# Optimization experiments

Hardware: AMD Instinct MI355X
Metric: run time of the kernel (lower is better)

## Reference

```python
import jax, jax.numpy as jnp
import numpy as np

B, T, C, H = 2, 2048, 1024, 16
HS = C // H

def setup_inputs() -> dict:
    key = jax.random.key(0)
    ks = jax.random.split(key, 5)
    s = 0.02
    return {
        "x": jax.random.normal(ks[0], (B, T, C), jnp.float32),
        "W_attn": jax.random.normal(ks[1], (C, 3 * C), jnp.float32) * s,
        "b_attn": jax.random.normal(ks[2], (3 * C,), jnp.float32) * s,
        "W_proj": jax.random.normal(ks[3], (C, C), jnp.float32) * s,
        "b_proj": jax.random.normal(ks[4], (C,), jnp.float32) * s,
    }

def reference(x, W_attn, b_attn, W_proj, b_proj):
    qkv = x @ W_attn + b_attn                      # [B,T,3C]
    q, k, v = jnp.split(qkv, 3, axis=-1)
    # [B,T,C] -> [B,H,T,hs]
    def heads(t):
        return t.reshape(B, T, H, HS).transpose(0, 2, 1, 3)
    q, k, v = heads(q), heads(k), heads(v)
    scale = 1.0 / jnp.sqrt(jnp.asarray(HS, x.dtype))
    attn = jnp.einsum('bhqd,bhkd->bhqk', q, k) * scale
    causal = jnp.tril(jnp.ones((T, T), bool))
    attn = jnp.where(causal[None, None], attn, -jnp.inf)
    attn = jax.nn.softmax(attn, axis=-1)
    y = jnp.einsum('bhqk,bhkd->bhqd', attn, v)
    y = y.transpose(0, 2, 1, 3).reshape(B, T, C)
    return y @ W_proj + b_proj
```

## Files before the change

### kernel.cpp

```cpp
#include <hip/hip_runtime.h>
#include <hip/hip_bf16.h>

static constexpr int Bn = 2, Tn = 2048, Cn = 1024, Hn = 16, HSn = 64;
static constexpr int Mrows = Bn * Tn;
static constexpr size_t PL = (size_t)Bn * Hn * Tn * HSn;

typedef __attribute__((ext_vector_type(8))) short short8;
typedef __attribute__((ext_vector_type(4))) float f32x4;

__device__ __forceinline__ unsigned short f2bf(float f) {
  __hip_bfloat16 h = __float2bfloat16(f);
  return *reinterpret_cast<unsigned short*>(&h);
}

__device__ __forceinline__ float fexp2(float x) {
  return __builtin_amdgcn_exp2f(x);
}

__device__ __forceinline__ void gload_lds16(const void* g, void* l) {
  __builtin_amdgcn_global_load_lds(
      (const __attribute__((address_space(1))) void*)g,
      (__attribute__((address_space(3))) void*)l, 16, 0, 0);
}

#define QSC 0.18033688011112042591999058512524f

__global__ __launch_bounds__(256) void prep_all(
    const float* __restrict__ x, unsigned short* __restrict__ xb,
    const float* __restrict__ Wa, unsigned short* __restrict__ Wab,
    const float* __restrict__ Wp, unsigned short* __restrict__ Wpb)
{
  const int bid = blockIdx.x, tid = threadIdx.x;
  if (bid < 4096) {
    int i = bid * 256 + tid;
    float4 v = ((const float4*)x)[i];
    ushort4 o;
    o.x = f2bf(v.x); o.y = f2bf(v.y); o.z = f2bf(v.z); o.w = f2bf(v.w);
    ((ushort4*)xb)[i] = o;
    return;
  }
  __shared__ float tile[32][33];
  const float* src; unsigned short* dst; int R, Cc, tb;
  if (bid < 4096 + 3072) { src = Wa; dst = Wab; R = Cn; Cc = 3 * Cn; tb = bid - 4096; }
  else                   { src = Wp; dst = Wpb; R = Cn; Cc = Cn;     tb = bid - 4096 - 3072; }
  const int nbx = Cc / 32;
  const int bx = tb % nbx, by = tb / nbx;
  const int tx = tid & 31, ty = tid >> 5;
  const int c0 = bx * 32, r0 = by * 32;
  #pragma unroll
  for (int i = 0; i < 4; ++i)
    tile[ty + 8 * i][tx] = src[(size_t)(r0 + ty + 8 * i) * Cc + c0 + tx];
  __syncthreads();
  #pragma unroll
  for (int i = 0; i < 4; ++i)
    dst[(size_t)(c0 + ty + 8 * i) * R + r0 + tx] = f2bf(tile[tx][ty + 8 * i]);
}

__global__ __launch_bounds__(512) void gemmQKV(
    const unsigned short* __restrict__ A, const unsigned short* __restrict__ Bt,
    const float* __restrict__ bias, unsigned short* __restrict__ qkv, int K)
{
  constexpr int NSTEP = 1024 / 64;
  constexpr int AF = 32;
  constexpr int BF = 24;
  __shared__ alignas(16) unsigned char lds[2][(AF + BF) * 1024];

  const int tid = threadIdx.x, wave = tid >> 6, lane = tid & 63;
  const int wr = wave >> 2, wc = wave & 3;
  const int orig = blockIdx.x;
  const int swz = (orig & 7) * 32 + (orig >> 3);
  const int bx = swz & 15, by = swz >> 4;
  const int tM = by * 256, tN = bx * 192;

  auto STAGE = [&](int buf, int k0) {
    #pragma unroll
    for (int i = 0; i < 7; ++i) {
      int f = wave * 7 + i;
      const unsigned short* g;
      int off;
      if (f < AF) {
        int mg = f >> 1, ks = f & 1;
        g = A + (size_t)(tM + mg * 16 + (lane & 15)) * K + k0 + ks * 32 + (lane >> 4) * 8;
        off = f * 1024;
      } else {
        int fg = f - AF;
        int ng = fg >> 1, ks = fg & 1;
        g = Bt + (size_t)(tN + ng * 16 + (lane & 15)) * K + k0 + ks * 32 + (lane >> 4) * 8;
        off = AF * 1024 + fg * 1024;
      }
      gload_lds16(g, &lds[buf][off]);
    }
  };

  f32x4 acc[8][3] = {};

  STAGE(0, 0);
  STAGE(1, 64);

  for (int t = 0; t < NSTEP; ++t) {
    if (t == NSTEP - 1)
      asm volatile("s_waitcnt vmcnt(0)" ::: "memory");
    else
      asm volatile("s_waitcnt vmcnt(7)" ::: "memory");
    __builtin_amdgcn_s_barrier();

    const int cur = t & 1;
    short8 af[8][2], bfr[3][2];
    #pragma unroll
    for (int ks = 0; ks < 2; ++ks) {
      #pragma unroll
      for (int m = 0; m < 8; ++m)
        af[m][ks] = *(const short8*)&lds[cur][((wr * 8 + m) * 2 + ks) * 1024 + lane * 16];
      #pragma unroll
      for (int n = 0; n < 3; ++n)
        bfr[n][ks] = *(const short8*)&lds[cur][AF * 1024 + ((wc * 3 + n) * 2 + ks) * 1024 + lane * 16];
    }
    asm volatile("s_waitcnt lgkmcnt(0)" ::: "memory");
    __builtin_amdgcn_sched_barrier(0);
    __builtin_amdgcn_s_barrier();

    if (t + 2 < NSTEP) STAGE(cur, (t + 2) * 64);

    __builtin_amdgcn_s_setprio(1);
    #pragma unroll
    for (int ks = 0; ks < 2; ++ks)
      #pragma unroll
      for (int m = 0; m < 8; ++m)
        #pragma unroll
        for (int n = 0; n < 3; ++n)
          acc[m][n] = __builtin_amdgcn_mfma_f32_16x16x32_bf16(af[m][ks], bfr[n][ks], acc[m][n], 0, 0, 0);
    __builtin_amdgcn_s_setprio(0);
  }

  const int a = lane & 15, hq = lane >> 4;
  #pragma unroll
  for (int m = 0; m < 8; ++m) {
    #pragma unroll
    for (int n = 0; n < 3; ++n) {
      int c = tN + wc * 48 + n * 16 + a;
      float bv = bias[c];
      int which = c >> 10;
      int cc = c & 1023, hh = cc >> 6, d = cc & 63;
      int row0 = tM + wr * 128 + m * 16 + hq * 4;
      int b = row0 >> 11, t0 = row0 & 2047;
      int bh = b * Hn + hh;
      if (which == 2) {
        ushort4 pk;
        pk.x = f2bf(acc[m][n][0] + bv);
        pk.y = f2bf(acc[m][n][1] + bv);
        pk.z = f2bf(acc[m][n][2] + bv);
        pk.w = f2bf(acc[m][n][3] + bv);
        *(ushort4*)&qkv[2 * PL + ((size_t)bh * HSn + d) * Tn + t0] = pk;
      } else {
        float sc = (which == 0) ? QSC : 1.0f;
        #pragma unroll
        for (int r = 0; r < 4; ++r) {
          float v = (acc[m][n][r] + bv) * sc;
          qkv[(size_t)which * PL + ((size_t)bh * Tn + t0 + r) * HSn + d] = f2bf(v);
        }
      }
    }
  }
}

template <int WM, int WN>
__global__ __launch_bounds__(256) void gemmP(
    const unsigned short* __restrict__ A, const unsigned short* __restrict__ Bt,
    const float* __restrict__ bias, float* __restrict__ O, int N, int K)
{
  constexpr int BM = WM * 32, BNt = WN * 32;
  constexpr int AF = BM / 16;
  constexpr int BF = BNt / 16;
  constexpr int NF = AF + BF;
  constexpr int PW = NF / 4;
  static_assert(PW == 3, "vmcnt literal");
  __shared__ alignas(16) unsigned char lds[2][NF * 1024];

  const int tid = threadIdx.x, wave = tid >> 6, lane = tid & 63;
  const int wr = wave >> 1, wc = wave & 1;
  const int orig = blockIdx.x;
  const int swz = (orig & 7) * 64 + (orig >> 3);
  const int bx = swz & 15, by = swz >> 4;
  const int tM = by * BM, tN = bx * BNt;

  auto STAGE = [&](int buf, int k0) {
    #pragma unroll
    for (int i = 0; i < PW; ++i) {
      int f = wave * PW + i;
      const unsigned short* g;
      if (f < AF)
        g = A + (size_t)(tM + f * 16 + (lane & 15)) * K + k0 + (lane >> 4) * 8;
      else
        g = Bt + (size_t)(tN + (f - AF) * 16 + (lane & 15)) * K + k0 + (lane >> 4) * 8;
      gload_lds16(g, &lds[buf][f * 1024]);
    }
  };

  f32x4 acc[WM][WN] = {};

  STAGE(0, 0);
  for (int t = 0, k0 = 0;; ++t, k0 += 32) {
    const int cur = t & 1;
    if (k0 + 32 < K) {
      STAGE(cur ^ 1, k0 + 32);
      asm volatile("s_waitcnt vmcnt(3)" ::: "memory");
    } else {
      asm volatile("s_waitcnt vmcnt(0)" ::: "memory");
    }
    __builtin_amdgcn_s_barrier();

    short8 af[WM], bfr[WN];
    #pragma unroll
    for (int m = 0; m < WM; ++m)
      af[m] = *(const short8*)&lds[cur][(wr * WM + m) * 1024 + lane * 16];
    #pragma unroll
    for (int n = 0; n < WN; ++n)
      bfr[n] = *(const short8*)&lds[cur][(AF + wc * WN + n) * 1024 + lane * 16];
    #pragma unroll
    for (int m = 0; m < WM; ++m)
      #pragma unroll
      for (int n = 0; n < WN; ++n)
        acc[m][n] = __builtin_amdgcn_mfma_f32_16x16x32_bf16(af[m], bfr[n], acc[m][n], 0, 0, 0);

    __builtin_amdgcn_s_barrier();
    if (k0 + 32 >= K) break;
  }

  const int a = lane & 15, hq = lane >> 4;
  #pragma unroll
  for (int m = 0; m < WM; ++m) {
    #pragma unroll
    for (int n = 0; n < WN; ++n) {
      int c = tN + wc * (WN * 16) + n * 16 + a;
      float bv = bias[c];
      int r0 = tM + wr * (WM * 16) + m * 16 + hq * 4;
      #pragma unroll
      for (int r = 0; r < 4; ++r)
        O[(size_t)(r0 + r) * N + c] = acc[m][n][r] + bv;
    }
  }
}

__global__ __launch_bounds__(256) void attn_mfma(
    const unsigned short* __restrict__ Qg, const unsigned short* __restrict__ Kg,
    const unsigned short* __restrict__ Vtg, unsigned short* __restrict__ Y)
{
  __shared__ alignas(16) unsigned char lds[41984];
  const int flat = blockIdx.x;
  const int logical = (flat & 7) * 64 + (flat >> 3);
  const int bh = logical >> 4;
  const int yb = logical & 15;
  const int tid = threadIdx.x, wave = tid >> 6, lane = tid & 63;
  const int a = lane & 15, h = lane >> 4;
  const unsigned short* Qp = Qg + (size_t)bh * Tn * HSn;
  const unsigned short* Kp = Kg + (size_t)bh * Tn * HSn;
  const unsigned short* Vp = Vtg + (size_t)bh * HSn * Tn;
  const int pbase = wave * 2304;
  const int qglob = wave * 16 + a;
  const int b = bh >> 4, hd = bh & 15;

  auto STAGE_K = [&](int kb, int kv0) {
    #pragma unroll
    for (int i = 0; i < 2; ++i) {
      int r8 = wave * 16 + i * 8;
      int row = r8 + (lane >> 3);
      int ch = (lane & 7) ^ (row & 7);
      gload_lds16(Kp + (size_t)(kv0 + row) * HSn + ch * 8,
                  &lds[9216 + kb * 8192 + r8 * 128]);
    }
  };
  auto STAGE_V = [&](int vb, int kv0) {
    #pragma unroll
    for (int i = 0; i < 2; ++i) {
      int r8 = wave * 16 + i * 8;
      int row = r8 + (lane >> 3);
      int ch = (lane & 7) ^ (row & 7);
      gload_lds16(Vp + (size_t)row * Tn + kv0 + ch * 8,
                  &lds[25600 + vb * 8192 + r8 * 128]);
    }
  };

  short8 ones;
  #pragma unroll
  for (int j = 0; j < 8; ++j) ones[j] = (short)0x3F80;

  for (int ph = 0; ph < 2; ++ph) {
    const int qt = ph ? (31 - yb) : yb;
    const int q0 = qt * 64;

    short8 qf[2];
    #pragma unroll
    for (int ks = 0; ks < 2; ++ks)
      qf[ks] = *(const short8*)(Qp + (size_t)(q0 + qglob) * HSn + ks * 32 + h * 8);

    STAGE_K(0, 0);
    STAGE_V(0, 0);
    if (qt >= 1) {
      STAGE_K(1, 64);
      STAGE_V(1, 64);
    }

    f32x4 o[4] = {};
    f32x4 lacc = {};

    for (int t = 0; t <= qt; ++t) {
      const int kb = t & 1;
      if (t == qt)
        asm volatile("s_waitcnt vmcnt(0)" ::: "memory");
      else
        asm volatile("s_waitcnt vmcnt(4)" ::: "memory");
      __builtin_amdgcn_s_barrier();

      const int kbase = 9216 + kb * 8192;
      const int vbase = 25600 + kb * 8192;

      f32x4 s[4] = {};
      __builtin_amdgcn_s_setprio(1);
      #pragma unroll
      for (int ks = 0; ks < 2; ++ks)
        #pragma unroll
        for (int n = 0; n < 4; ++n) {
          int kr = n * 16 + a;
          int ch = (ks * 4 + h) ^ (kr & 7);
          short8 kf = *(const short8*)&lds[kbase + kr * 128 + ch * 16];
          s[n] = __builtin_amdgcn_mfma_f32_16x16x32_bf16(kf, qf[ks], s[n], 0, 0, 0);
        }
      __builtin_amdgcn_s_setprio(0);

      if (t == qt) {
        #pragma unroll
        for (int n = 0; n < 4; ++n)
          #pragma unroll
          for (int r = 0; r < 4; ++r)
            if ((n * 16 + h * 4 + r) > qglob) s[n][r] = -1e30f;
      }

      #pragma unroll
      for (int n = 0; n < 4; ++n)
        #pragma unroll
        for (int r = 0; r < 4; ++r) s[n][r] = fexp2(s[n][r]);

      #pragma unroll
      for (int n = 0; n < 4; ++n) {
        uint2 w2;
        w2.x = (unsigned)f2bf(s[n][0]) | ((unsigned)f2bf(s[n][1]) << 16);
        w2.y = (unsigned)f2bf(s[n][2]) | ((unsigned)f2bf(s[n][3]) << 16);
        *(uint2*)&lds[pbase + (a * 36 + n * 8 + h * 2) * 4] = w2;
      }

      __builtin_amdgcn_s_setprio(1);
      #pragma unroll
      for (int ks = 0; ks < 2; ++ks) {
        short8 pa = *(const short8*)&lds[pbase + (a * 36 + ks * 16 + h * 4) * 4];
        lacc = __builtin_amdgcn_mfma_f32_16x16x32_bf16(pa, ones, lacc, 0, 0, 0);
        #pragma unroll
        for (int n = 0; n < 4; ++n) {
          int d = n * 16 + a;
          int ch = (ks * 4 + h) ^ (d & 7);
          short8 vf = *(const short8*)&lds[vbase + d * 128 + ch * 16];
          o[n] = __builtin_amdgcn_mfma_f32_16x16x32_bf16(pa, vf, o[n], 0, 0, 0);
        }
      }
      __builtin_amdgcn_s_setprio(0);

      __builtin_amdgcn_s_barrier();
      if (t + 2 <= qt) {
        STAGE_K(kb, (t + 2) * 64);
        STAGE_V(kb, (t + 2) * 64);
      }
    }

    f32x4 inv;
    #pragma unroll
    for (int r = 0; r < 4; ++r) inv[r] = 1.0f / lacc[r];
    #pragma unroll
    for (int n = 0; n < 4; ++n)
      #pragma unroll
      for (int r = 0; r < 4; ++r) {
        int tr = q0 + wave * 16 + 4 * h + r;
        int col = hd * 64 + n * 16 + a;
        Y[((size_t)(b * Tn + tr)) * Cn + col] = f2bf(o[n][r] * inv[r]);
      }
  }
}

extern "C" void kernel_launch(void* const* d_in, const int* in_sizes, int n_in,
                              void* d_out, int out_size, void* d_ws, size_t ws_size,
                              hipStream_t stream) {
  const float* x      = (const float*)d_in[0];
  const float* W_attn = (const float*)d_in[1];
  const float* b_attn = (const float*)d_in[2];
  const float* W_proj = (const float*)d_in[3];
  const float* b_proj = (const float*)d_in[4];
  float* out = (float*)d_out;

  unsigned short* xb  = (unsigned short*)d_ws;
  unsigned short* Wab = xb + (size_t)Mrows * Cn;
  unsigned short* Wpb = Wab + (size_t)3 * Cn * Cn;
  unsigned short* qkv = Wpb + (size_t)Cn * Cn;
  unsigned short* y   = qkv + 3 * PL;

  prep_all<<<4096 + 3072 + 1024, 256, 0, stream>>>(x, xb, W_attn, Wab, W_proj, Wpb);

  gemmQKV<<<256, 512, 0, stream>>>(xb, Wab, b_attn, qkv, Cn);

  attn_mfma<<<512, 256, 0, stream>>>(qkv, qkv + PL, qkv + 2 * PL, y);

  gemmP<4, 2><<<512, 256, 0, stream>>>(y, Wpb, b_proj, out, Cn, Cn);
}
```

Before: 109.3 us.

## Fuse all four stages into one persistent kernel with grid barriers

Replaces the four separate launches (conversion/transpose, QKV GEMM, attention, projection GEMM) with a single persistent kernel of 256 blocks of 512 threads, separated by software grid barriers built on atomics. Attention and projection stages pack two former 256-thread blocks into each 512-thread block using separate LDS halves. The aim is to remove kernel launch gaps and tail effects between stages. In exchange it adds a memset launch, spin-wait barriers that rely on all 256 blocks being co-resident, and only one block per CU via launch bounds and large LDS, which may reduce latency hiding in the attention and projection phases.

New measurement: 390.3 us. 257% more time.

```diff
diff --git a/kernel.cpp b/kernel.cpp
--- a/kernel.cpp
+++ b/kernel.cpp
@@ -25,362 +25,372 @@
 
 #define QSC 0.18033688011112042591999058512524f
 
-__global__ __launch_bounds__(256) void prep_all(
-    const float* __restrict__ x, unsigned short* __restrict__ xb,
-    const float* __restrict__ Wa, unsigned short* __restrict__ Wab,
-    const float* __restrict__ Wp, unsigned short* __restrict__ Wpb)
+__device__ __forceinline__ void grid_barrier(unsigned* bar, int slot) {
+  __threadfence();
+  __syncthreads();
+  if (threadIdx.x == 0) {
+    atomicAdd(&bar[slot], 1u);
+    while (atomicAdd(&bar[slot], 0u) < 256u) __builtin_amdgcn_s_sleep(8);
+  }
+  __syncthreads();
+  __threadfence();
+}
+
+__global__ __launch_bounds__(512, 1) void fused_all(
+    const float* __restrict__ x,
+    const float* __restrict__ Wa, const float* __restrict__ ba,
+    const float* __restrict__ Wp, const float* __restrict__ bp,
+    unsigned short* __restrict__ xb, unsigned short* __restrict__ Wab,
+    unsigned short* __restrict__ Wpb, unsigned short* __restrict__ qkv,
+    unsigned short* __restrict__ y, float* __restrict__ out,
+    unsigned* __restrict__ bar)
 {
-  const int bid = blockIdx.x, tid = threadIdx.x;
-  if (bid < 4096) {
-    int i = bid * 256 + tid;
-    float4 v = ((const float4*)x)[i];
-    ushort4 o;
-    o.x = f2bf(v.x); o.y = f2bf(v.y); o.z = f2bf(v.z); o.w = f2bf(v.w);
-    ((ushort4*)xb)[i] = o;
-    return;
+  __shared__ alignas(16) unsigned char lds[114688];
+  const int blk = blockIdx.x, tid = threadIdx.x;
+  const int wave = tid >> 6, lane = tid & 63;
+  const int a = lane & 15, h = lane >> 4;
+
+  {
+    const float4* xs = (const float4*)x;
+    ushort4* xd = (ushort4*)xb;
+    for (int i = blk * 512 + tid; i < Mrows * Cn / 4; i += 256 * 512) {
+      float4 v = xs[i];
+      ushort4 o;
+      o.x = f2bf(v.x); o.y = f2bf(v.y); o.z = f2bf(v.z); o.w = f2bf(v.w);
+      xd[i] = o;
+    }
+    float* tile = (float*)(lds + (tid >> 8) * 4224);
+    const int t256 = tid & 255;
+    const int tx = t256 & 31, ty = t256 >> 5;
+    for (int pass = 0; pass < 8; ++pass) {
+      int tb = blk * 16 + pass * 2 + (tid >> 8);
+      const float* src; unsigned short* dst; int Cc, tnum;
+      if (tb < 3072) { src = Wa; dst = Wab; Cc = 3 * Cn; tnum = tb; }
+      else           { src = Wp; dst = Wpb; Cc = Cn;     tnum = tb - 3072; }
+      const int nbx = Cc / 32;
+      const int bx = tnum % nbx, by = tnum / nbx;
+      const int c0 = bx * 32, r0 = by * 32;
+      #pragma unroll
+      for (int i = 0; i < 4; ++i)
+        tile[(ty + 8 * i) * 33 + tx] = src[(size_t)(r0 + ty + 8 * i) * Cc + c0 + tx];
+      __syncthreads();
+      #pragma unroll
+      for (int i = 0; i < 4; ++i)
+        dst[(size_t)(c0 + ty + 8 * i) * Cn + r0 + tx] = f2bf(tile[tx * 33 + ty + 8 * i]);
+      __syncthreads();
+    }
   }
-  __shared__ float tile[32][33];
-  const float* src; unsigned short* dst; int R, Cc, tb;
-  if (bid < 4096 + 3072) { src = Wa; dst = Wab; R = Cn; Cc = 3 * Cn; tb = bid - 4096; }
-  else                   { src = Wp; dst = Wpb; R = Cn; Cc = Cn;     tb = bid - 4096 - 3072; }
-  const int nbx = Cc / 32;
-  const int bx = tb % nbx, by = tb / nbx;
-  const int tx = tid & 31, ty = tid >> 5;
-  const int c0 = bx * 32, r0 = by * 32;
-  #pragma unroll
-  for (int i = 0; i < 4; ++i)
-    tile[ty + 8 * i][tx] = src[(size_t)(r0 + ty + 8 * i) * Cc + c0 + tx];
-  __syncthreads();
-  #pragma unroll
-  for (int i = 0; i < 4; ++i)
-    dst[(size_t)(c0 + ty + 8 * i) * R + r0 + tx] = f2bf(tile[tx][ty + 8 * i]);
-}
-
-__global__ __launch_bounds__(512) void gemmQKV(
-    const unsigned short* __restrict__ A, const unsigned short* __restrict__ Bt,
-    const float* __restrict__ bias, unsigned short* __restrict__ qkv, int K)
-{
-  constexpr int NSTEP = 1024 / 64;
-  constexpr int AF = 32;
-  constexpr int BF = 24;
-  __shared__ alignas(16) unsigned char lds[2][(AF + BF) * 1024];
-
-  const int tid = threadIdx.x, wave = tid >> 6, lane = tid & 63;
-  const int wr = wave >> 2, wc = wave & 3;
-  const int orig = blockIdx.x;
-  const int swz = (orig & 7) * 32 + (orig >> 3);
-  const int bx = swz & 15, by = swz >> 4;
-  const int tM = by * 256, tN = bx * 192;
-
-  auto STAGE = [&](int buf, int k0) {
-    #pragma unroll
-    for (int i = 0; i < 7; ++i) {
-      int f = wave * 7 + i;
-      const unsigned short* g;
-      int off;
-      if (f < AF) {
-        int mg = f >> 1, ks = f & 1;
-        g = A + (size_t)(tM + mg * 16 + (lane & 15)) * K + k0 + ks * 32 + (lane >> 4) * 8;
-        off = f * 1024;
-      } else {
-        int fg = f - AF;
-        int ng = fg >> 1, ks = fg & 1;
-        g = Bt + (size_t)(tN + ng * 16 + (lane & 15)) * K + k0 + ks * 32 + (lane >> 4) * 8;
-        off = AF * 1024 + fg * 1024;
-      }
-      gload_lds16(g, &lds[buf][off]);
-    }
-  };
-
-  f32x4 acc[8][3] = {};
-
-  STAGE(0, 0);
-  STAGE(1, 64);
-
-  for (int t = 0; t < NSTEP; ++t) {
-    if (t == NSTEP - 1)
-      asm volatile("s_waitcnt vmcnt(0)" ::: "memory");
-    else
-      asm volatile("s_waitcnt vmcnt(7)" ::: "memory");
-    __builtin_amdgcn_s_barrier();
-
-    const int cur = t & 1;
-    short8 af[8][2], bfr[3][2];
-    #pragma unroll
-    for (int ks = 0; ks < 2; ++ks) {
-      #pragma unroll
-      for (int m = 0; m < 8; ++m)
-        af[m][ks] = *(const short8*)&lds[cur][((wr * 8 + m) * 2 + ks) * 1024 + lane * 16];
-      #pragma unroll
-      for (int n = 0; n < 3; ++n)
-        bfr[n][ks] = *(const short8*)&lds[cur][AF * 1024 + ((wc * 3 + n) * 2 + ks) * 1024 + lane * 16];
-    }
-    asm volatile("s_waitcnt lgkmcnt(0)" ::: "memory");
-    __builtin_amdgcn_sched_barrier(0);
-    __builtin_amdgcn_s_barrier();
-
-    if (t + 2 < NSTEP) STAGE(cur, (t + 2) * 64);
-
-    __builtin_amdgcn_s_setprio(1);
-    #pragma unroll
-    for (int ks = 0; ks < 2; ++ks)
-      #pragma unroll
-      for (int m = 0; m < 8; ++m)
-        #pragma unroll
-        for (int n = 0; n < 3; ++n)
-          acc[m][n] = __builtin_amdgcn_mfma_f32_16x16x32_bf16(af[m][ks], bfr[n][ks], acc[m][n], 0, 0, 0);
-    __builtin_amdgcn_s_setprio(0);
-  }
-
-  const int a = lane & 15, hq = lane >> 4;
-  #pragma unroll
-  for (int m = 0; m < 8; ++m) {
-    #pragma unroll
-    for (int n = 0; n < 3; ++n) {
-      int c = tN + wc * 48 + n * 16 + a;
-      float bv = bias[c];
-      int which = c >> 10;
-      int cc = c & 1023, hh = cc >> 6, d = cc & 63;
-      int row0 = tM + wr * 128 + m * 16 + hq * 4;
-      int b = row0 >> 11, t0 = row0 & 2047;
-      int bh = b * Hn + hh;
-      if (which == 2) {
-        ushort4 pk;
-        pk.x = f2bf(acc[m][n][0] + bv);
-        pk.y = f2bf(acc[m][n][1] + bv);
-        pk.z = f2bf(acc[m][n][2] + bv);
-        pk.w = f2bf(acc[m][n][3] + bv);
-        *(ushort4*)&qkv[2 * PL + ((size_t)bh * HSn + d) * Tn + t0] = pk;
-      } else {
-        float sc = (which == 0) ? QSC : 1.0f;
-        #pragma unroll
-        for (int r = 0; r < 4; ++r) {
-          float v = (acc[m][n][r] + bv) * sc;
-          qkv[(size_t)which * PL + ((size_t)bh * Tn + t0 + r) * HSn + d] = f2bf(v);
-        }
-      }
-    }
-  }
-}
-
-template <int WM, int WN>
-__global__ __launch_bounds__(256) void gemmP(
-    const unsigned short* __restrict__ A, const unsigned short* __restrict__ Bt,
-    const float* __restrict__ bias, float* __restrict__ O, int N, int K)
-{
-  constexpr int BM = WM * 32, BNt = WN * 32;
-  constexpr int AF = BM / 16;
-  constexpr int BF = BNt / 16;
-  constexpr int NF = AF + BF;
-  constexpr int PW = NF / 4;
-  static_assert(PW == 3, "vmcnt literal");
-  __shared__ alignas(16) unsigned char lds[2][NF * 1024];
-
-  const int tid = threadIdx.x, wave = tid >> 6, lane = tid & 63;
-  const int wr = wave >> 1, wc = wave & 1;
-  const int orig = blockIdx.x;
-  const int swz = (orig & 7) * 64 + (orig >> 3);
-  const int bx = swz & 15, by = swz >> 4;
-  const int tM = by * BM, tN = bx * BNt;
-
-  auto STAGE = [&](int buf, int k0) {
-    #pragma unroll
-    for (int i = 0; i < PW; ++i) {
-      int f = wave * PW + i;
-      const unsigned short* g;
-      if (f < AF)
-        g = A + (size_t)(tM + f * 16 + (lane & 15)) * K + k0 + (lane >> 4) * 8;
-      else
-        g = Bt + (size_t)(tN + (f - AF) * 16 + (lane & 15)) * K + k0 + (lane >> 4) * 8;
-      gload_lds16(g, &lds[buf][f * 1024]);
-    }
-  };
-
-  f32x4 acc[WM][WN] = {};
-
-  STAGE(0, 0);
-  for (int t = 0, k0 = 0;; ++t, k0 += 32) {
-    const int cur = t & 1;
-    if (k0 + 32 < K) {
-      STAGE(cur ^ 1, k0 + 32);
-      asm volatile("s_waitcnt vmcnt(3)" ::: "memory");
-    } else {
-      asm volatile("s_waitcnt vmcnt(0)" ::: "memory");
-    }
-    __builtin_amdgcn_s_barrier();
-
-    short8 af[WM], bfr[WN];
-    #pragma unroll
-    for (int m = 0; m < WM; ++m)
-      af[m] = *(const short8*)&lds[cur][(wr * WM + m) * 1024 + lane * 16];
-    #pragma unroll
-    for (int n = 0; n < WN; ++n)
-      bfr[n] = *(const short8*)&lds[cur][(AF + wc * WN + n) * 1024 + lane * 16];
-    #pragma unroll
-    for (int m = 0; m < WM; ++m)
-      #pragma unroll
-      for (int n = 0; n < WN; ++n)
-        acc[m][n] = __builtin_amdgcn_mfma_f32_16x16x32_bf16(af[m], bfr[n], acc[m][n], 0, 0, 0);
-
-    __builtin_amdgcn_s_barrier();
-    if (k0 + 32 >= K) break;
-  }
-
-  const int a = lane & 15, hq = lane >> 4;
-  #pragma unroll
-  for (int m = 0; m < WM; ++m) {
-    #pragma unroll
-    for (int n = 0; n < WN; ++n) {
-      int c = tN + wc * (WN * 16) + n * 16 + a;
-      float bv = bias[c];
-      int r0 = tM + wr * (WM * 16) + m * 16 + hq * 4;
-      #pragma unroll
-      for (int r = 0; r < 4; ++r)
-        O[(size_t)(r0 + r) * N + c] = acc[m][n][r] + bv;
-    }
-  }
-}
-
-__global__ __launch_bounds__(256) void attn_mfma(
-    const unsigned short* __restrict__ Qg, const unsigned short* __restrict__ Kg,
-    const unsigned short* __restrict__ Vtg, unsigned short* __restrict__ Y)
-{
-  __shared__ alignas(16) unsigned char lds[41984];
-  const int flat = blockIdx.x;
-  const int logical = (flat & 7) * 64 + (flat >> 3);
-  const int bh = logical >> 4;
-  const int yb = logical & 15;
-  const int tid = threadIdx.x, wave = tid >> 6, lane = tid & 63;
-  const int a = lane & 15, h = lane >> 4;
-  const unsigned short* Qp = Qg + (size_t)bh * Tn * HSn;
-  const unsigned short* Kp = Kg + (size_t)bh * Tn * HSn;
-  const unsigned short* Vp = Vtg + (size_t)bh * HSn * Tn;
-  const int pbase = wave * 2304;
-  const int qglob = wave * 16 + a;
-  const int b = bh >> 4, hd = bh & 15;
-
-  auto STAGE_K = [&](int kb, int kv0) {
-    #pragma unroll
-    for (int i = 0; i < 2; ++i) {
-      int r8 = wave * 16 + i * 8;
-      int row = r8 + (lane >> 3);
-      int ch = (lane & 7) ^ (row & 7);
-      gload_lds16(Kp + (size_t)(kv0 + row) * HSn + ch * 8,
-                  &lds[9216 + kb * 8192 + r8 * 128]);
-    }
-  };
-  auto STAGE_V = [&](int vb, int kv0) {
-    #pragma unroll
-    for (int i = 0; i < 2; ++i) {
-      int r8 = wave * 16 + i * 8;
-      int row = r8 + (lane >> 3);
-      int ch = (lane & 7) ^ (row & 7);
-      gload_lds16(Vp + (size_t)row * Tn + kv0 + ch * 8,
-                  &lds[25600 + vb * 8192 + r8 * 128]);
-    }
-  };
-
-  short8 ones;
-  #pragma unroll
-  for (int j = 0; j < 8; ++j) ones[j] = (short)0x3F80;
-
-  for (int ph = 0; ph < 2; ++ph) {
-    const int qt = ph ? (31 - yb) : yb;
-    const int q0 = qt * 64;
-
-    short8 qf[2];
-    #pragma unroll
-    for (int ks = 0; ks < 2; ++ks)
-      qf[ks] = *(const short8*)(Qp + (size_t)(q0 + qglob) * HSn + ks * 32 + h * 8);
-
-    STAGE_K(0, 0);
-    STAGE_V(0, 0);
-    if (qt >= 1) {
-      STAGE_K(1, 64);
-      STAGE_V(1, 64);
-    }
-
-    f32x4 o[4] = {};
-    f32x4 lacc = {};
-
-    for (int t = 0; t <= qt; ++t) {
-      const int kb = t & 1;
-      if (t == qt)
+  grid_barrier(bar, 0);
+
+  {
+    constexpr int NSTEP = 16;
+    constexpr int AF = 32, BF = 24;
+    const int wr = wave >> 2, wc = wave & 3;
+    const int swz = (blk & 7) * 32 + (blk >> 3);
+    const int bx = swz & 15, by = swz >> 4;
+    const int tM = by * 256, tN = bx * 192;
+    const int K = Cn;
+
+    auto STAGE = [&](int buf, int k0) {
+      #pragma unroll
+      for (int i = 0; i < 7; ++i) {
+        int f = wave * 7 + i;
+        const unsigned short* g;
+        int off;
+        if (f < AF) {
+          int mg = f >> 1, ks = f & 1;
+          g = xb + (size_t)(tM + mg * 16 + (lane & 15)) * K + k0 + ks * 32 + (lane >> 4) * 8;
+          off = f * 1024;
+        } else {
+          int fg = f - AF;
+          int ng = fg >> 1, ks = fg & 1;
+          g = Wab + (size_t)(tN + ng * 16 + (lane & 15)) * K + k0 + ks * 32 + (lane >> 4) * 8;
+          off = AF * 1024 + fg * 1024;
+        }
+        gload_lds16(g, &lds[buf * 57344 + off]);
+      }
+    };
+
+    f32x4 acc[8][3] = {};
+
+    STAGE(0, 0);
+    STAGE(1, 64);
+
+    for (int t = 0; t < NSTEP; ++t) {
+      if (t == NSTEP - 1)
         asm volatile("s_waitcnt vmcnt(0)" ::: "memory");
       else
-        asm volatile("s_waitcnt vmcnt(4)" ::: "memory");
+        asm volatile("s_waitcnt vmcnt(7)" ::: "memory");
       __builtin_amdgcn_s_barrier();
 
-      const int kbase = 9216 + kb * 8192;
-      const int vbase = 25600 + kb * 8192;
-
-      f32x4 s[4] = {};
+      const int cur = t & 1;
+      const unsigned char* base = &lds[cur * 57344];
+      short8 af[8][2], bfr[3][2];
+      #pragma unroll
+      for (int ks = 0; ks < 2; ++ks) {
+        #pragma unroll
+        for (int m = 0; m < 8; ++m)
+          af[m][ks] = *(const short8*)&base[((wr * 8 + m) * 2 + ks) * 1024 + lane * 16];
+        #pragma unroll
+        for (int n = 0; n < 3; ++n)
+          bfr[n][ks] = *(const short8*)&base[AF * 1024 + ((wc * 3 + n) * 2 + ks) * 1024 + lane * 16];
+      }
+      asm volatile("s_waitcnt lgkmcnt(0)" ::: "memory");
+      __builtin_amdgcn_sched_barrier(0);
+      __builtin_amdgcn_s_barrier();
+
+      if (t + 2 < NSTEP) STAGE(cur, (t + 2) * 64);
+
       __builtin_amdgcn_s_setprio(1);
       #pragma unroll
       for (int ks = 0; ks < 2; ++ks)
         #pragma unroll
+        for (int m = 0; m < 8; ++m)
+          #pragma unroll
+          for (int n = 0; n < 3; ++n)
+            acc[m][n] = __builtin_amdgcn_mfma_f32_16x16x32_bf16(af[m][ks], bfr[n][ks], acc[m][n], 0, 0, 0);
+      __builtin_amdgcn_s_setprio(0);
+    }
+
+    const int hq = lane >> 4;
+    #pragma unroll
+    for (int m = 0; m < 8; ++m) {
+      #pragma unroll
+      for (int n = 0; n < 3; ++n) {
+        int c = tN + wc * 48 + n * 16 + a;
+        float bv = ba[c];
+        int which = c >> 10;
+        int cc = c & 1023, hh = cc >> 6, d = cc & 63;
+        int row0 = tM + wr * 128 + m * 16 + hq * 4;
+        int b = row0 >> 11, t0 = row0 & 2047;
+        int bh = b * Hn + hh;
+        if (which == 2) {
+          ushort4 pk;
+          pk.x = f2bf(acc[m][n][0] + bv);
+          pk.y = f2bf(acc[m][n][1] + bv);
+          pk.z = f2bf(acc[m][n][2] + bv);
+          pk.w = f2bf(acc[m][n][3] + bv);
+          *(ushort4*)&qkv[2 * PL + ((size_t)bh * HSn + d) * Tn + t0] = pk;
+        } else {
+          float sc = (which == 0) ? QSC : 1.0f;
+          #pragma unroll
+          for (int r = 0; r < 4; ++r) {
+            float v = (acc[m][n][r] + bv) * sc;
+            qkv[(size_t)which * PL + ((size_t)bh * Tn + t0 + r) * HSn + d] = f2bf(v);
+          }
+        }
+      }
+    }
+  }
+  grid_barrier(bar, 1);
+
+  {
+    const int yb = blk & 15;
+    const int half = wave >> 2;
+    const int bh = ((blk >> 4) << 1) | half;
+    const int w4 = wave & 3;
+    unsigned char* L = lds + half * 41984;
+    const unsigned short* Qp = qkv + (size_t)bh * Tn * HSn;
+    const unsigned short* Kp = qkv + PL + (size_t)bh * Tn * HSn;
+    const unsigned short* Vp = qkv + 2 * PL + (size_t)bh * HSn * Tn;
+    const int pbase = w4 * 2304;
+    const int qglob = w4 * 16 + a;
+    const int b = bh >> 4, hd = bh & 15;
+
+    auto STAGE_K = [&](int kb, int kv0) {
+      #pragma unroll
+      for (int i = 0; i < 2; ++i) {
+        int r8 = w4 * 16 + i * 8;
+        int row = r8 + (lane >> 3);
+        int ch = (lane & 7) ^ (row & 7);
+        gload_lds16(Kp + (size_t)(kv0 + row) * HSn + ch * 8,
+                    &L[9216 + kb * 8192 + r8 * 128]);
+      }
+    };
+    auto STAGE_V = [&](int vb, int kv0) {
+      #pragma unroll
+      for (int i = 0; i < 2; ++i) {
+        int r8 = w4 * 16 + i * 8;
+        int row = r8 + (lane >> 3);
+        int ch = (lane & 7) ^ (row & 7);
+        gload_lds16(Vp + (size_t)row * Tn + kv0 + ch * 8,
+                    &L[25600 + vb * 8192 + r8 * 128]);
+      }
+    };
+
+    short8 ones;
+    #pragma unroll
+    for (int j = 0; j < 8; ++j) ones[j] = (short)0x3F80;
+
+    for (int ph = 0; ph < 2; ++ph) {
+      const int qt = ph ? (31 - yb) : yb;
+      const int q0 = qt * 64;
+
+      short8 qf[2];
+      #pragma unroll
+      for (int ks = 0; ks < 2; ++ks)
+        qf[ks] = *(const short8*)(Qp + (size_t)(q0 + qglob) * HSn + ks * 32 + h * 8);
+
+      STAGE_K(0, 0);
+      STAGE_V(0, 0);
+      if (qt >= 1) {
+        STAGE_K(1, 64);
+        STAGE_V(1, 64);
+      }
+
+      f32x4 o[4] = {};
+      f32x4 lacc = {};
+
+      for (int t = 0; t <= qt; ++t) {
+        const int kb = t & 1;
+        if (t == qt)
+          asm volatile("s_waitcnt vmcnt(0)" ::: "memory");
+        else
+          asm volatile("s_waitcnt vmcnt(4)" ::: "memory");
+        __builtin_amdgcn_s_barrier();
+
+        const int kbase = 9216 + kb * 8192;
+        const int vbase = 25600 + kb * 8192;
+
+        f32x4 s[4] = {};
+        __builtin_amdgcn_s_setprio(1);
+        #pragma unroll
+        for (int ks = 0; ks < 2; ++ks)
+          #pragma unroll
+          for (int n = 0; n < 4; ++n) {
+            int kr = n * 16 + a;
+            int ch = (ks * 4 + h) ^ (kr & 7);
+            short8 kf = *(const short8*)&L[kbase + kr * 128 + ch * 16];
+            s[n] = __builtin_amdgcn_mfma_f32_16x16x32_bf16(kf, qf[ks], s[n], 0, 0, 0);
+          }
+        __builtin_amdgcn_s_setprio(0);
+
+        if (t == qt) {
+          #pragma unroll
+          for (int n = 0; n < 4; ++n)
+            #pragma unroll
+            for (int r = 0; r < 4; ++r)
+              if ((n * 16 + h * 4 + r) > qglob) s[n][r] = -1e30f;
+        }
+
+        #pragma unroll
+        for (int n = 0; n < 4; ++n)
+          #pragma unroll
+          for (int r = 0; r < 4; ++r) s[n][r] = fexp2(s[n][r]);
+
+        #pragma unroll
         for (int n = 0; n < 4; ++n) {
-          int kr = n * 16 + a;
-          int ch = (ks * 4 + h) ^ (kr & 7);
-          short8 kf = *(const short8*)&lds[kbase + kr * 128 + ch * 16];
-          s[n] = __builtin_amdgcn_mfma_f32_16x16x32_bf16(kf, qf[ks], s[n], 0, 0, 0);
-        }
-      __builtin_amdgcn_s_setprio(0);
-
-      if (t == qt) {
-        #pragma unroll
-        for (int n = 0; n < 4; ++n)
-          #pragma unroll
-          for (int r = 0; r < 4; ++r)
-            if ((n * 16 + h * 4 + r) > qglob) s[n][r] = -1e30f;
-      }
-
+          uint2 w2;
+          w2.x = (unsigned)f2bf(s[n][0]) | ((unsigned)f2bf(s[n][1]) << 16);
+          w2.y = (unsigned)f2bf(s[n][2]) | ((unsigned)f2bf(s[n][3]) << 16);
+          *(uint2*)&L[pbase + (a * 36 + n * 8 + h * 2) * 4] = w2;
+        }
+
+        __builtin_amdgcn_s_setprio(1);
+        #pragma unroll
+        for (int ks = 0; ks < 2; ++ks) {
+          short8 pa = *(const short8*)&L[pbase + (a * 36 + ks * 16 + h * 4) * 4];
+          lacc = __builtin_amdgcn_mfma_f32_16x16x32_bf16(pa, ones, lacc, 0, 0, 0);
+          #pragma unroll
+          for (int n = 0; n < 4; ++n) {
+            int d = n * 16 + a;
+            int ch = (ks * 4 + h) ^ (d & 7);
+            short8 vf = *(const short8*)&L[vbase + d * 128 + ch * 16];
+            o[n] = __builtin_amdgcn_mfma_f32_16x16x32_bf16(pa, vf, o[n], 0, 0, 0);
+          }
+        }
+        __builtin_amdgcn_s_setprio(0);
+
+        __builtin_amdgcn_s_barrier();
+        if (t + 2 <= qt) {
+          STAGE_K(kb, (t + 2) * 64);
+          STAGE_V(kb, (t + 2) * 64);
+        }
+      }
+
+      f32x4 inv;
+      #pragma unroll
+      for (int r = 0; r < 4; ++r) inv[r] = 1.0f / lacc[r];
       #pragma unroll
       for (int n = 0; n < 4; ++n)
         #pragma unroll
-        for (int r = 0; r < 4; ++r) s[n][r] = fexp2(s[n][r]);
-
-      #pragma unroll
-      for (int n = 0; n < 4; ++n) {
-        uint2 w2;
-        w2.x = (unsigned)f2bf(s[n][0]) | ((unsigned)f2bf(s[n][1]) << 16);
-        w2.y = (unsigned)f2bf(s[n][2]) | ((unsigned)f2bf(s[n][3]) << 16);
-        *(uint2*)&lds[pbase + (a * 36 + n * 8 + h * 2) * 4] = w2;
-      }
-
-      __builtin_amdgcn_s_setprio(1);
-      #pragma unroll
-      for (int ks = 0; ks < 2; ++ks) {
-        short8 pa = *(const short8*)&lds[pbase + (a * 36 + ks * 16 + h * 4) * 4];
-        lacc = __builtin_amdgcn_mfma_f32_16x16x32_bf16(pa, ones, lacc, 0, 0, 0);
-        #pragma unroll
-        for (int n = 0; n < 4; ++n) {
-          int d = n * 16 + a;
-          int ch = (ks * 4 + h) ^ (d & 7);
-          short8 vf = *(const short8*)&lds[vbase + d * 128 + ch * 16];
-          o[n] = __builtin_amdgcn_mfma_f32_16x16x32_bf16(pa, vf, o[n], 0, 0, 0);
-        }
-      }
-      __builtin_amdgcn_s_setprio(0);
-
+        for (int r = 0; r < 4; ++r) {
+          int tr = q0 + w4 * 16 + 4 * h + r;
+          int col = hd * 64 + n * 16 + a;
+          y[((size_t)(b * Tn + tr)) * Cn + col] = f2bf(o[n][r] * inv[r]);
+        }
+    }
+  }
+  grid_barrier(bar, 2);
+
+  {
+    constexpr int AF = 8, BF = 4;
+    const int bx = blk & 15;
+    const int half = wave >> 2;
+    const int by = ((blk >> 4) << 1) | half;
+    const int w4 = wave & 3;
+    const int wr = w4 >> 1, wc = w4 & 1;
+    unsigned char* L = lds + half * 24576;
+    const int tM = by * 128, tN = bx * 64;
+    const int K = Cn;
+
+    auto STAGE = [&](int buf, int k0) {
+      #pragma unroll
+      for (int i = 0; i < 3; ++i) {
+        int f = w4 * 3 + i;
+        const unsigned short* g;
+        if (f < AF)
+          g = y + (size_t)(tM + f * 16 + (lane & 15)) * K + k0 + (lane >> 4) * 8;
+        else
+          g = Wpb + (size_t)(tN + (f - AF) * 16 + (lane & 15)) * K + k0 + (lane >> 4) * 8;
+        gload_lds16(g, &L[buf * 12288 + f * 1024]);
+      }
+    };
+
+    f32x4 acc[4][2] = {};
+
+    STAGE(0, 0);
+    for (int t = 0, k0 = 0;; ++t, k0 += 32) {
+      const int cur = t & 1;
+      if (k0 + 32 < K) {
+        STAGE(cur ^ 1, k0 + 32);
+        asm volatile("s_waitcnt vmcnt(3)" ::: "memory");
+      } else {
+        asm volatile("s_waitcnt vmcnt(0)" ::: "memory");
+      }
       __builtin_amdgcn_s_barrier();
-      if (t + 2 <= qt) {
-        STAGE_K(kb, (t + 2) * 64);
-        STAGE_V(kb, (t + 2) * 64);
-      }
-    }
-
-    f32x4 inv;
+
+      const unsigned char* base = &L[cur * 12288];
+      short8 af[4], bfr[2];
+      #pragma unroll
+      for (int m = 0; m < 4; ++m)
+        af[m] = *(const short8*)&base[(wr * 4 + m) * 1024 + lane * 16];
+      #pragma unroll
+      for (int n = 0; n < 2; ++n)
+        bfr[n] = *(const short8*)&base[(AF + wc * 2 + n) * 1024 + lane * 16];
+      #pragma unroll
+      for (int m = 0; m < 4; ++m)
+        #pragma unroll
+        for (int n = 0; n < 2; ++n)
+          acc[m][n] = __builtin_amdgcn_mfma_f32_16x16x32_bf16(af[m], bfr[n], acc[m][n], 0, 0, 0);
+
+      __builtin_amdgcn_s_barrier();
+      if (k0 + 32 >= K) break;
+    }
+
+    const int hq = lane >> 4;
     #pragma unroll
-    for (int r = 0; r < 4; ++r) inv[r] = 1.0f / lacc[r];
-    #pragma unroll
-    for (int n = 0; n < 4; ++n)
-      #pragma unroll
-      for (int r = 0; r < 4; ++r) {
-        int tr = q0 + wave * 16 + 4 * h + r;
-        int col = hd * 64 + n * 16 + a;
-        Y[((size_t)(b * Tn + tr)) * Cn + col] = f2bf(o[n][r] * inv[r]);
-      }
+    for (int m = 0; m < 4; ++m) {
+      #pragma unroll
+      for (int n = 0; n < 2; ++n) {
+        int c = tN + wc * 32 + n * 16 + a;
+        float bv = bp[c];
+        int r0 = tM + wr * 64 + m * 16 + hq * 4;
+        #pragma unroll
+        for (int r = 0; r < 4; ++r)
+          out[(size_t)(r0 + r) * Cn + c] = acc[m][n][r] + bv;
+      }
+    }
   }
 }
 
@@ -399,12 +409,11 @@
   unsigned short* Wpb = Wab + (size_t)3 * Cn * Cn;
   unsigned short* qkv = Wpb + (size_t)Cn * Cn;
   unsigned short* y   = qkv + 3 * PL;
-
-  prep_all<<<4096 + 3072 + 1024, 256, 0, stream>>>(x, xb, W_attn, Wab, W_proj, Wpb);
-
-  gemmQKV<<<256, 512, 0, stream>>>(xb, Wab, b_attn, qkv, Cn);
-
-  attn_mfma<<<512, 256, 0, stream>>>(qkv, qkv + PL, qkv + 2 * PL, y);
-
-  gemmP<4, 2><<<512, 256, 0, stream>>>(y, Wpb, b_proj, out, Cn, Cn);
-}
+  unsigned* bar       = (unsigned*)(y + (size_t)Mrows * Cn);
+
+  hipMemsetAsync(bar, 0, 4 * sizeof(unsigned), stream);
+
+  fused_all<<<256, 512, 0, stream>>>(
+      x, W_attn, b_attn, W_proj, b_proj,
+      xb, Wab, Wpb, qkv, y, out, bar);
+}
```
